# Kernel tuning notes

Measured on AMD Instinct MI355X. Metric: run time of the kernel, lower is better.

Reference implementation:

```python
import jax, jax.numpy as jnp
import numpy as np

B, T, D, H, NH = 128, 64, 64, 128, 4


def setup_inputs() -> dict:
    key = jax.random.key(0)
    ks = jax.random.split(key, 32)
    s = 0.05
    inp = {
        "x": jax.random.normal(ks[0], (B, T, D), dtype=jnp.float32),
        "mask": jnp.ones((B, T), dtype=jnp.int32),
        # per-feature GRU params (input size 1, PyTorch gate order r,z,n)
        "Wih": jax.random.normal(ks[1], (D, 3 * H), dtype=jnp.float32) * s,
        "Whh": jax.random.normal(ks[2], (D, 3 * H, H), dtype=jnp.float32) * s,
        "bih": jax.random.normal(ks[3], (D, 3 * H), dtype=jnp.float32) * s,
        "bhh": jax.random.normal(ks[4], (D, 3 * H), dtype=jnp.float32) * s,
        # MHA projections (stored [in,out]; y = x @ W + b)
        "Wq": jax.random.normal(ks[5], (H, H), dtype=jnp.float32) * s,
        "bq": jnp.zeros((H,), dtype=jnp.float32),
        "Wk": jax.random.normal(ks[6], (H, H), dtype=jnp.float32) * s,
        "bk": jnp.zeros((H,), dtype=jnp.float32),
        "Wv": jax.random.normal(ks[7], (H, H), dtype=jnp.float32) * s,
        "bv": jnp.zeros((H,), dtype=jnp.float32),
        "Wo": jax.random.normal(ks[8], (H, H), dtype=jnp.float32) * s,
        "bo": jnp.zeros((H,), dtype=jnp.float32),
        # FFN
        "W1": jax.random.normal(ks[9], (H, 2 * H), dtype=jnp.float32) * s,
        "b1": jnp.zeros((2 * H,), dtype=jnp.float32),
        "W2": jax.random.normal(ks[10], (2 * H, H), dtype=jnp.float32) * s,
        "b2": jnp.zeros((H,), dtype=jnp.float32),
        # LayerNorms
        "g1": jnp.ones((H,), dtype=jnp.float32),
        "be1": jnp.zeros((H,), dtype=jnp.float32),
        "g2": jnp.ones((H,), dtype=jnp.float32),
        "be2": jnp.zeros((H,), dtype=jnp.float32),
        # FinalAttentionQKV
        "Fq": jax.random.normal(ks[11], (H, H), dtype=jnp.float32) * s,
        "fbq": jnp.zeros((H,), dtype=jnp.float32),
        "Fk": jax.random.normal(ks[12], (H, H), dtype=jnp.float32) * s,
        "fbk": jnp.zeros((H,), dtype=jnp.float32),
        "Fv": jax.random.normal(ks[13], (H, H), dtype=jnp.float32) * s,
        "fbv": jnp.zeros((H,), dtype=jnp.float32),
        "Fout": jax.random.normal(ks[14], (H,), dtype=jnp.float32) * s,
        "fbout": jnp.zeros((), dtype=jnp.float32),
    }
    return inp


def _layernorm(x, g, b, eps=1e-5):
    m = jnp.mean(x, axis=-1, keepdims=True)
    v = jnp.mean((x - m) ** 2, axis=-1, keepdims=True)
    return (x - m) * jax.lax.rsqrt(v + eps) * g + b


def _forward(x, mask, Wih, Whh, bih, bhh, Wq, bq, Wk, bk, Wv, bv, Wo, bo,
             W1, b1, W2, b2, g1, be1, g2, be2,
             Fq, fbq, Fk, fbk, Fv, fbv, Fout, fbout):
    Bc, Tc, Dc = x.shape
    Hc = Whh.shape[-1]

    # --- D independent GRUs, fused: batch axes (B, D), scalar input per step ---
    def step(h, xt):  # h: [B,D,H], xt: [B,D]
        gx = xt[..., None] * Wih + bih                     # [B,D,3H]
        gh = jnp.einsum('bdh,dkh->bdk', h, Whh) + bhh      # [B,D,3H]
        r = jax.nn.sigmoid(gx[..., :Hc] + gh[..., :Hc])
        z = jax.nn.sigmoid(gx[..., Hc:2 * Hc] + gh[..., Hc:2 * Hc])
        n = jnp.tanh(gx[..., 2 * Hc:] + r * gh[..., 2 * Hc:])
        hn = (1.0 - z) * n + z * h
        return hn, hn

    xs = jnp.transpose(x, (1, 0, 2))                        # [T,B,D]
    h0 = jnp.zeros((Bc, Dc, Hc), dtype=x.dtype)
    _, ys = jax.lax.scan(step, h0, xs)                      # [T,B,D,H]

    # last_by_lengths: gather hidden state at index lengths-1 per batch element
    lengths = jnp.sum(mask, axis=1)                         # [B]
    idx = jnp.clip(lengths - 1, 0, Tc - 1)
    emb = ys[idx, jnp.arange(Bc)]                           # [B,D,H] (D tokens)

    # --- MHA (self-attention over D feature tokens); dropout = identity (eval) ---
    dk = Hc // NH
    def split_heads(t):
        return jnp.transpose(t.reshape(Bc, Dc, NH, dk), (0, 2, 1, 3))  # [B,NH,D,dk]
    q = split_heads(emb @ Wq + bq)
    k = split_heads(emb @ Wk + bk)
    v = split_heads(emb @ Wv + bv)
    scores = jnp.einsum('bhnd,bhmd->bhnm', q, k) / jnp.sqrt(jnp.float32(dk))
    attn = jax.nn.softmax(scores, axis=-1)
    o = jnp.einsum('bhnm,bhmd->bhnd', attn, v)
    o = jnp.transpose(o, (0, 2, 1, 3)).reshape(Bc, Dc, Hc)
    mha_out = o @ Wo + bo

    h1 = _layernorm(emb + mha_out, g1, be1)
    ffn = jax.nn.relu(h1 @ W1 + b1) @ W2 + b2
    h2 = _layernorm(h1 + ffn, g2, be2)

    # --- FinalAttentionQKV ---
    fq = (h2[:, -1, :] @ Fq + fbq)[:, None, :]              # [B,1,H]
    fk = h2 @ Fk + fbk                                      # [B,D,H]
    fv = h2 @ Fv + fbv                                      # [B,D,H]
    e = jnp.tanh(fq + fk) @ Fout + fbout                    # [B,D]
    a = jax.nn.softmax(e, axis=-1)
    return jnp.einsum('bn,bnh->bh', a, fv)                  # [B,H]


def reference(x, mask, Wih, Whh, bih, bhh, Wq, bq, Wk, bk, Wv, bv, Wo, bo,
              W1, b1, W2, b2, g1, be1, g2, be2,
              Fq, fbq, Fk, fbk, Fv, fbv, Fout, fbout):
    return _forward(x, mask, Wih, Whh, bih, bhh, Wq, bq, Wk, bk, Wv, bv, Wo, bo,
                    W1, b1, W2, b2, g1, be1, g2, be2,
                    Fq, fbq, Fk, fbk, Fv, fbv, Fout, fbout)
```

## Files before the change

kernel.cpp:

```cpp
#include <hip/hip_runtime.h>
#include <hip/hip_bf16.h>
#include <math.h>

#define BB 128
#define TT 64
#define DD 64
#define HH 128
#define NHH 4
#define K3H 384

typedef __attribute__((ext_vector_type(8))) short short8_t;
typedef __attribute__((ext_vector_type(4))) float float4_t;

#define LOG2E 1.4426950408889634f

__device__ __forceinline__ unsigned short f2bf(float f) {
    unsigned int u = __float_as_uint(f);
    u += 0x7fffu + ((u >> 16) & 1u);
    return (unsigned short)(u >> 16);
}

__device__ __forceinline__ unsigned pack_bf2(float lo, float hi) {
    return (unsigned)f2bf(lo) | ((unsigned)f2bf(hi) << 16);
}

__device__ __forceinline__ unsigned pack_bf2_hw(float lo, float hi) {
    __hip_bfloat162 p = __float22bfloat162_rn(make_float2(lo, hi));
    unsigned u;
    __builtin_memcpy(&u, &p, 4);
    return u;
}

__device__ __forceinline__ float bf2f(unsigned short s) {
    return __uint_as_float((unsigned)s << 16);
}

__device__ __forceinline__ float2 pk_fma(float2 a, float2 b, float2 c) {
    return make_float2(fmaf(a.x, b.x, c.x), fmaf(a.y, b.y, c.y));
}
__device__ __forceinline__ float2 pk_sub(float2 a, float2 b) {
    return make_float2(a.x - b.x, a.y - b.y);
}

__device__ __forceinline__ void gru_epilogue(
    const float4_t& ar, const float4_t& az, const float4_t& an, float xv,
    const float wrs[4], const float wzs[4], const float wns[4],
    const float bnis[4], float hprev[4], float hn4[4])
{
    float2 xv2 = make_float2(xv, xv);
#pragma unroll
    for (int pp = 0; pp < 2; ++pp) {
        const int r0 = 2 * pp, r1 = r0 + 1;
        float2 grs = pk_fma(xv2, make_float2(wrs[r0], wrs[r1]),
                            make_float2(ar[r0], ar[r1]));
        float2 gzs = pk_fma(xv2, make_float2(wzs[r0], wzs[r1]),
                            make_float2(az[r0], az[r1]));
        float2 rg = make_float2(
            __builtin_amdgcn_rcpf(1.f + __builtin_amdgcn_exp2f(grs.x)),
            __builtin_amdgcn_rcpf(1.f + __builtin_amdgcn_exp2f(grs.y)));
        float2 gns = pk_fma(rg, make_float2(an[r0], an[r1]),
                            pk_fma(xv2, make_float2(wns[r0], wns[r1]),
                                   make_float2(bnis[r0], bnis[r1])));
        float2 t1 = make_float2(1.f + __builtin_amdgcn_exp2f(gns.x),
                                1.f + __builtin_amdgcn_exp2f(gns.y));
        float2 t2 = make_float2(1.f + __builtin_amdgcn_exp2f(gzs.x),
                                1.f + __builtin_amdgcn_exp2f(gzs.y));
        float2 iD = make_float2(__builtin_amdgcn_rcpf(t1.x * t2.x),
                                __builtin_amdgcn_rcpf(t1.y * t2.y));
        float2 tn = make_float2(fmaf(-2.f, t2.x * iD.x, 1.f),
                                fmaf(-2.f, t2.y * iD.y, 1.f));
        float2 zg = make_float2(t1.x * iD.x, t1.y * iD.y);
        float2 hp = make_float2(hprev[r0], hprev[r1]);
        float2 hn = pk_fma(zg, pk_sub(hp, tn), tn);
        hprev[r0] = hn.x; hprev[r1] = hn.y;
        hn4[r0] = hn.x; hn4[r1] = hn.y;
    }
}

__global__ __launch_bounds__(512, 2) void gru_mfma_kernel(
    const float* __restrict__ x, const int* __restrict__ mask,
    const float* __restrict__ Wih, const float* __restrict__ Whh,
    const float* __restrict__ bih, const float* __restrict__ bhh,
    float* __restrict__ emb)
{
    const int d  = blockIdx.x;
    const int b0 = blockIdx.y * 32;
    const int tid = threadIdx.x;
    const int w = tid >> 6;
    const int l = tid & 63;
    const int m = l & 15;
    const int q = l >> 4;

    __shared__ __align__(16) unsigned short hbuf[2][2][16][144];
    __shared__ float xs_t[TT][32];
    __shared__ int tstar_s[32];
    __shared__ char lds_pad_[30 * 1024];
    if (mask[0] == 0x7abcdef) ((volatile char*)lds_pad_)[0] = 1;

    for (int idx = tid; idx < 32 * TT; idx += 512) {
        int t = idx >> 5, row = idx & 31;
        xs_t[t][row] = x[((size_t)(b0 + row) * TT + t) * DD + d];
    }
    if (tid < 32) {
        int b = b0 + tid, len = 0;
        for (int t = 0; t < TT; ++t) len += mask[b * TT + t];
        int ts = len - 1;
        if (ts < 0) ts = 0;
        if (ts > TT - 1) ts = TT - 1;
        tstar_s[tid] = ts;
    }
    for (int idx = tid; idx < 2 * 2 * 16 * 144; idx += 512)
        ((unsigned short*)hbuf)[idx] = 0;

    short8_t Wf[3][4];
#pragma unroll
    for (int g = 0; g < 3; ++g) {
        float sc = (g == 2) ? (2.f * LOG2E) : (-LOG2E);
        int kcol = g * HH + 16 * w + m;
        const float* wrow = Whh + ((size_t)d * K3H + kcol) * HH;
#pragma unroll
        for (int kc = 0; kc < 4; ++kc) {
            int j0 = kc * 32 + q * 8;
            float4 w0 = *(const float4*)(wrow + j0);
            float4 w1 = *(const float4*)(wrow + j0 + 4);
            short8_t f;
            f[0] = (short)f2bf(w0.x * sc); f[1] = (short)f2bf(w0.y * sc);
            f[2] = (short)f2bf(w0.z * sc); f[3] = (short)f2bf(w0.w * sc);
            f[4] = (short)f2bf(w1.x * sc); f[5] = (short)f2bf(w1.y * sc);
            f[6] = (short)f2bf(w1.z * sc); f[7] = (short)f2bf(w1.w * sc);
            Wf[g][kc] = f;
        }
    }

    const int hcol0 = 16 * w + q * 4;
    float4 wr4 = *(const float4*)&Wih[d * K3H + hcol0];
    float4 wz4 = *(const float4*)&Wih[d * K3H + HH + hcol0];
    float4 wn4 = *(const float4*)&Wih[d * K3H + 2 * HH + hcol0];
    float4 br4 = *(const float4*)&bih[d * K3H + hcol0];
    float4 bz4 = *(const float4*)&bih[d * K3H + HH + hcol0];
    float4 bni4 = *(const float4*)&bih[d * K3H + 2 * HH + hcol0];
    float4 bhr4 = *(const float4*)&bhh[d * K3H + hcol0];
    float4 bhz4 = *(const float4*)&bhh[d * K3H + HH + hcol0];
    float4 bnh4 = *(const float4*)&bhh[d * K3H + 2 * HH + hcol0];
    float brs[4], bzs[4], bnis[4], bnhs[4], wrs[4], wzs[4], wns[4];
#pragma unroll
    for (int r = 0; r < 4; ++r) {
        wrs[r] = -LOG2E * ((const float*)&wr4)[r];
        wzs[r] = -LOG2E * ((const float*)&wz4)[r];
        wns[r] = 2.f * LOG2E * ((const float*)&wn4)[r];
        brs[r] = -LOG2E * (((const float*)&br4)[r] + ((const float*)&bhr4)[r]);
        bzs[r] = -LOG2E * (((const float*)&bz4)[r] + ((const float*)&bhz4)[r]);
        bnis[r] = 2.f * LOG2E * ((const float*)&bni4)[r];
        bnhs[r] = 2.f * LOG2E * ((const float*)&bnh4)[r];
    }

    float hprevA[4], hprevB[4];
#pragma unroll
    for (int i = 0; i < 4; ++i) { hprevA[i] = 0.f; hprevB[i] = 0.f; }

    __syncthreads();
    const int tstarA = tstar_s[m];
    const int tstarB = tstar_s[16 + m];
    float* embpA = emb + (((size_t)(b0 + m)) * DD + d) * HH + hcol0;
    float* embpB = emb + (((size_t)(b0 + 16 + m)) * DD + d) * HH + hcol0;

    for (int t = 0; t < TT; ++t) {
        const int par = t & 1;

        short8_t hfA[4], hfB[4];
#pragma unroll
        for (int kc = 0; kc < 4; ++kc) {
            hfA[kc] = *(const short8_t*)&hbuf[0][par][m][kc * 32 + q * 8];
            hfB[kc] = *(const short8_t*)&hbuf[1][par][m][kc * 32 + q * 8];
        }
        float xvA = xs_t[t][m];
        float xvB = xs_t[t][16 + m];

        float4_t arA = {brs[0], brs[1], brs[2], brs[3]};
        float4_t azA = {bzs[0], bzs[1], bzs[2], bzs[3]};
        float4_t anA = {bnhs[0], bnhs[1], bnhs[2], bnhs[3]};
        float4_t arB = arA, azB = azA, anB = anA;
#pragma unroll
        for (int kc = 0; kc < 4; ++kc) {
            arA = __builtin_amdgcn_mfma_f32_16x16x32_bf16(Wf[0][kc], hfA[kc], arA, 0, 0, 0);
            azA = __builtin_amdgcn_mfma_f32_16x16x32_bf16(Wf[1][kc], hfA[kc], azA, 0, 0, 0);
            anA = __builtin_amdgcn_mfma_f32_16x16x32_bf16(Wf[2][kc], hfA[kc], anA, 0, 0, 0);
        }
#pragma unroll
        for (int kc = 0; kc < 4; ++kc) {
            arB = __builtin_amdgcn_mfma_f32_16x16x32_bf16(Wf[0][kc], hfB[kc], arB, 0, 0, 0);
            azB = __builtin_amdgcn_mfma_f32_16x16x32_bf16(Wf[1][kc], hfB[kc], azB, 0, 0, 0);
            anB = __builtin_amdgcn_mfma_f32_16x16x32_bf16(Wf[2][kc], hfB[kc], anB, 0, 0, 0);
        }

        float hn4[4];
        gru_epilogue(arA, azA, anA, xvA, wrs, wzs, wns, bnis, hprevA, hn4);
        {
            uint2 uu;
            uu.x = pack_bf2_hw(hn4[0], hn4[1]);
            uu.y = pack_bf2_hw(hn4[2], hn4[3]);
            *(uint2*)&hbuf[0][par ^ 1][m][hcol0] = uu;
            if (t == tstarA) {
                float4 hv; hv.x = hn4[0]; hv.y = hn4[1]; hv.z = hn4[2]; hv.w = hn4[3];
                *(float4*)embpA = hv;
            }
        }
        gru_epilogue(arB, azB, anB, xvB, wrs, wzs, wns, bnis, hprevB, hn4);
        {
            uint2 uu;
            uu.x = pack_bf2_hw(hn4[0], hn4[1]);
            uu.y = pack_bf2_hw(hn4[2], hn4[3]);
            *(uint2*)&hbuf[1][par ^ 1][m][hcol0] = uu;
            if (t == tstarB) {
                float4 hv; hv.x = hn4[0]; hv.y = hn4[1]; hv.z = hn4[2]; hv.w = hn4[3];
                *(float4*)embpB = hv;
            }
        }
        __syncthreads();
    }
}

__device__ __forceinline__ void load_wfrag(const float* __restrict__ Wp, int N,
                                           int col, float scale, int q,
                                           short8_t fr[4])
{
#pragma unroll
    for (int kc = 0; kc < 4; ++kc) {
        const float* p = Wp + (size_t)(kc * 32 + q * 8) * N + col;
        short8_t f;
#pragma unroll
        for (int j = 0; j < 8; ++j)
            f[j] = (short)f2bf(p[(size_t)j * N] * scale);
        fr[kc] = f;
    }
}

__device__ __forceinline__ void load_afrag(const unsigned short (*S)[136],
                                           short8_t Af[4][4], int m16, int q)
{
#pragma unroll
    for (int mt = 0; mt < 4; ++mt)
#pragma unroll
        for (int kc = 0; kc < 4; ++kc)
            Af[mt][kc] = *(const short8_t*)&S[mt * 16 + m16][kc * 32 + q * 8];
}

__device__ __forceinline__ void mm_regw(short8_t Af[4][4], short8_t Bf[4],
                                        float4_t acc[4])
{
#pragma unroll
    for (int mt = 0; mt < 4; ++mt) {
        float4_t a = acc[mt];
#pragma unroll
        for (int kc = 0; kc < 4; ++kc)
            a = __builtin_amdgcn_mfma_f32_16x16x32_bf16(Af[mt][kc], Bf[kc], a, 0, 0, 0);
        acc[mt] = a;
    }
}

__device__ __forceinline__ void zero4(float4_t acc[4]) {
#pragma unroll
    for (int mt = 0; mt < 4; ++mt) acc[mt] = (float4_t){0.f, 0.f, 0.f, 0.f};
}

__device__ __forceinline__ void store_rows(unsigned short (*Dst)[136], float4_t acc[4],
                                           float bv, int relu, int col, int q)
{
#pragma unroll
    for (int mt = 0; mt < 4; ++mt)
#pragma unroll
        for (int reg = 0; reg < 4; ++reg) {
            float v = acc[mt][reg] + bv;
            if (relu) v = fmaxf(v, 0.f);
            Dst[mt * 16 + q * 4 + reg][col] = f2bf(v);
        }
}

__global__ __launch_bounds__(512) void tail_kernel(
    const float* __restrict__ emb,
    const float* __restrict__ Wq, const float* __restrict__ bq,
    const float* __restrict__ Wk, const float* __restrict__ bk,
    const float* __restrict__ Wv, const float* __restrict__ bv,
    const float* __restrict__ Wo, const float* __restrict__ bo,
    const float* __restrict__ W1, const float* __restrict__ b1,
    const float* __restrict__ W2, const float* __restrict__ b2,
    const float* __restrict__ g1, const float* __restrict__ be1,
    const float* __restrict__ g2, const float* __restrict__ be2,
    const float* __restrict__ Fq, const float* __restrict__ fbq,
    const float* __restrict__ Fk, const float* __restrict__ fbk,
    const float* __restrict__ Fv, const float* __restrict__ fbv,
    const float* __restrict__ Fout, const float* __restrict__ fbout,
    float* __restrict__ out)
{
    const int b = blockIdx.x;
    const int tid = threadIdx.x;
    const int w = tid >> 6, l = tid & 63, m16 = l & 15, q = l >> 4;
    const int col = w * 16 + m16;

    __shared__ __align__(16) unsigned short E[64][136];
    __shared__ __align__(16) unsigned short Qs[64][136];
    __shared__ __align__(16) unsigned short Ks[64][136];
    __shared__ __align__(16) unsigned short Vt[128][72];
    __shared__ float sc4[4][64][66];
    __shared__ float lnp[64][8], lnp2[64][8];
    __shared__ float mean_s[64], rs_s[64];
    __shared__ float fq_s[128], fo_s[128], e_s[64], red_s[256];

    const float* embB = emb + (size_t)b * 64 * 128;
    const float SS = 0.17677669529663687f;

    short8_t WqF[4], WkF[4], WvF[4];
    load_wfrag(Wq, 128, col, SS, q, WqF);
    load_wfrag(Wk, 128, col, 1.f, q, WkF);
    load_wfrag(Wv, 128, col, 1.f, q, WvF);
    float bqv = bq[col] * SS, bkv = bk[col], bvv = bv[col];

    for (int it = tid; it < 2048; it += 512) {
        int r = it >> 5, c4 = (it & 31) << 2;
        float4 a = *(const float4*)&embB[r * 128 + c4];
        uint2 p; p.x = pack_bf2(a.x, a.y); p.y = pack_bf2(a.z, a.w);
        *(uint2*)&E[r][c4] = p;
    }
    __syncthreads();

    short8_t Af[4][4];
    float4_t acc[4];
    load_afrag(E, Af, m16, q);

    zero4(acc); mm_regw(Af, WqF, acc); store_rows(Qs, acc, bqv, 0, col, q);
    zero4(acc); mm_regw(Af, WkF, acc); store_rows(Ks, acc, bkv, 0, col, q);
    zero4(acc); mm_regw(Af, WvF, acc);
#pragma unroll
    for (int mt = 0; mt < 4; ++mt) {
        uint2 pk;
        pk.x = pack_bf2(acc[mt][0] + bvv, acc[mt][1] + bvv);
        pk.y = pack_bf2(acc[mt][2] + bvv, acc[mt][3] + bvv);
        *(uint2*)&Vt[col][mt * 16 + q * 4] = pk;
    }
    __syncthreads();

    short8_t WoF[4], W1aF[4], W1bF[4];
    load_wfrag(Wo, 128, col, 1.f, q, WoF);
    load_wfrag(W1, 256, col, 1.f, q, W1aF);
    load_wfrag(W1, 256, 128 + col, 1.f, q, W1bF);
    float bov = bo[col], b1a = b1[col], b1b = b1[128 + col];
    float g1v = g1[col], be1v = be1[col];

    {
        int hd = w >> 1, ntb = (w & 1) * 2;
#pragma unroll
        for (int mt = 0; mt < 4; ++mt) {
            short8_t Aq = *(const short8_t*)&Qs[mt * 16 + m16][hd * 32 + q * 8];
#pragma unroll
            for (int nn = 0; nn < 2; ++nn) {
                int nt = ntb + nn;
                short8_t Bk = *(const short8_t*)&Ks[nt * 16 + m16][hd * 32 + q * 8];
                float4_t a = {0.f, 0.f, 0.f, 0.f};
                a = __builtin_amdgcn_mfma_f32_16x16x32_bf16(Aq, Bk, a, 0, 0, 0);
#pragma unroll
                for (int reg = 0; reg < 4; ++reg)
                    sc4[hd][mt * 16 + q * 4 + reg][nt * 16 + m16] = a[reg];
            }
        }
    }
    __syncthreads();

    {
        int pr = tid >> 1, hd2 = pr >> 6, row = pr & 63, half = (tid & 1) * 32;
        float v[32]; float mx = -1e30f;
#pragma unroll
        for (int c = 0; c < 32; ++c) { v[c] = sc4[hd2][row][half + c]; mx = fmaxf(mx, v[c]); }
        mx = fmaxf(mx, __shfl_xor(mx, 1));
        float sum = 0.f;
#pragma unroll
        for (int c = 0; c < 32; ++c) { v[c] = __expf(v[c] - mx); sum += v[c]; }
        sum += __shfl_xor(sum, 1);
        float inv = __builtin_amdgcn_rcpf(sum);
        unsigned short (*Pd)[136] = (hd2 < 2) ? Qs : Ks;
        int cb = (hd2 & 1) * 64 + half;
#pragma unroll
        for (int c = 0; c < 16; ++c)
            *(unsigned*)&Pd[row][cb + 2 * c] = pack_bf2(v[2 * c] * inv, v[2 * c + 1] * inv);
    }
    __syncthreads();

    {
        int hd = w >> 1, nt = w & 1;
        const unsigned short (*P)[136] = (hd < 2) ? (const unsigned short (*)[136])Qs
                                                  : (const unsigned short (*)[136])Ks;
        int pb = (hd & 1) * 64;
        int vrow = hd * 32 + nt * 16 + m16;
        short8_t B0f = *(const short8_t*)&Vt[vrow][q * 8];
        short8_t B1f = *(const short8_t*)&Vt[vrow][32 + q * 8];
#pragma unroll
        for (int mt = 0; mt < 4; ++mt) {
            short8_t A0 = *(const short8_t*)&P[mt * 16 + m16][pb + q * 8];
            short8_t A1 = *(const short8_t*)&P[mt * 16 + m16][pb + 32 + q * 8];
            float4_t a = {0.f, 0.f, 0.f, 0.f};
            a = __builtin_amdgcn_mfma_f32_16x16x32_bf16(A0, B0f, a, 0, 0, 0);
            a = __builtin_amdgcn_mfma_f32_16x16x32_bf16(A1, B1f, a, 0, 0, 0);
#pragma unroll
            for (int reg = 0; reg < 4; ++reg)
                E[mt * 16 + q * 4 + reg][vrow] = f2bf(a[reg]);
        }
    }
    __syncthreads();

    short8_t W2aF[4], W2bF[4], FkF[4], FvF[4];
    load_wfrag(W2, 128, col, 1.f, q, W2aF);
    load_wfrag(W2 + (size_t)128 * 128, 128, col, 1.f, q, W2bF);
    load_wfrag(Fk, 128, col, 1.f, q, FkF);
    load_wfrag(Fv, 128, col, 1.f, q, FvF);
    float b2v = b2[col], fbkv = fbk[col], fbvv = fbv[col];
    float g2v = g2[col], be2v = be2[col];

    load_afrag(E, Af, m16, q);
    zero4(acc); mm_regw(Af, WoF, acc);
    float h1v[4][4];
#pragma unroll
    for (int mt = 0; mt < 4; ++mt)
#pragma unroll
        for (int reg = 0; reg < 4; ++reg) {
            int row = mt * 16 + q * 4 + reg;
            h1v[mt][reg] = acc[mt][reg] + bov + embB[(size_t)row * 128 + col];
        }
#pragma unroll
    for (int mt = 0; mt < 4; ++mt)
#pragma unroll
        for (int reg = 0; reg < 4; ++reg) {
            float s = h1v[mt][reg], s2 = s * s;
            s += __shfl_xor(s, 1); s += __shfl_xor(s, 2); s += __shfl_xor(s, 4); s += __shfl_xor(s, 8);
            s2 += __shfl_xor(s2, 1); s2 += __shfl_xor(s2, 2); s2 += __shfl_xor(s2, 4); s2 += __shfl_xor(s2, 8);
            if (m16 == 0) { int row = mt * 16 + q * 4 + reg; lnp[row][w] = s; lnp2[row][w] = s2; }
        }
    __syncthreads();
    if (tid < 64) {
        float s = 0.f, s2 = 0.f;
#pragma unroll
        for (int k = 0; k < 8; ++k) { s += lnp[tid][k]; s2 += lnp2[tid][k]; }
        float mn = s * (1.f / 128.f);
        mean_s[tid] = mn;
        rs_s[tid] = rsqrtf(s2 * (1.f / 128.f) - mn * mn + 1e-5f);
    }
    __syncthreads();
#pragma unroll
    for (int mt = 0; mt < 4; ++mt)
#pragma unroll
        for (int reg = 0; reg < 4; ++reg) {
            int row = mt * 16 + q * 4 + reg;
            float hv = (h1v[mt][reg] - mean_s[row]) * rs_s[row] * g1v + be1v;
            h1v[mt][reg] = hv;
            E[row][col] = f2bf(hv);
        }
    __syncthreads();

    load_afrag(E, Af, m16, q);
    zero4(acc); mm_regw(Af, W1aF, acc); store_rows(Qs, acc, b1a, 1, col, q);
    zero4(acc); mm_regw(Af, W1bF, acc); store_rows(Ks, acc, b1b, 1, col, q);
    __syncthreads();

    {
        short8_t AfQ[4][4], AfK[4][4];
        load_afrag(Qs, AfQ, m16, q);
        load_afrag(Ks, AfK, m16, q);
        zero4(acc); mm_regw(AfQ, W2aF, acc); mm_regw(AfK, W2bF, acc);
    }
#pragma unroll
    for (int mt = 0; mt < 4; ++mt)
#pragma unroll
        for (int reg = 0; reg < 4; ++reg)
            h1v[mt][reg] = acc[mt][reg] + b2v + h1v[mt][reg];
#pragma unroll
    for (int mt = 0; mt < 4; ++mt)
#pragma unroll
        for (int reg = 0; reg < 4; ++reg) {
            float s = h1v[mt][reg], s2 = s * s;
            s += __shfl_xor(s, 1); s += __shfl_xor(s, 2); s += __shfl_xor(s, 4); s += __shfl_xor(s, 8);
            s2 += __shfl_xor(s2, 1); s2 += __shfl_xor(s2, 2); s2 += __shfl_xor(s2, 4); s2 += __shfl_xor(s2, 8);
            if (m16 == 0) { int row = mt * 16 + q * 4 + reg; lnp[row][w] = s; lnp2[row][w] = s2; }
        }
    __syncthreads();
    if (tid < 64) {
        float s = 0.f, s2 = 0.f;
#pragma unroll
        for (int k = 0; k < 8; ++k) { s += lnp[tid][k]; s2 += lnp2[tid][k]; }
        float mn = s * (1.f / 128.f);
        mean_s[tid] = mn;
        rs_s[tid] = rsqrtf(s2 * (1.f / 128.f) - mn * mn + 1e-5f);
    }
    __syncthreads();
#pragma unroll
    for (int mt = 0; mt < 4; ++mt)
#pragma unroll
        for (int reg = 0; reg < 4; ++reg) {
            int row = mt * 16 + q * 4 + reg;
            float hv = (h1v[mt][reg] - mean_s[row]) * rs_s[row] * g2v + be2v;
            E[row][col] = f2bf(hv);
        }
    __syncthreads();

    load_afrag(E, Af, m16, q);
    zero4(acc); mm_regw(Af, FkF, acc); store_rows(Qs, acc, fbkv, 0, col, q);
    zero4(acc); mm_regw(Af, FvF, acc); store_rows(Ks, acc, fbvv, 0, col, q);
    {
        int co = tid >> 2, sub = tid & 3;
        float a2 = 0.f;
#pragma unroll 8
        for (int mm2 = sub * 32; mm2 < sub * 32 + 32; ++mm2)
            a2 = fmaf(bf2f(E[63][mm2]), Fq[(size_t)mm2 * 128 + co], a2);
        a2 += __shfl_xor(a2, 1);
        a2 += __shfl_xor(a2, 2);
        if (sub == 0) fq_s[co] = a2 + fbq[co];
    }
    if (tid < 128) fo_s[tid] = Fout[tid];
    __syncthreads();

    {
        int dd = tid >> 3, c8 = tid & 7;
        float p = 0.f;
#pragma unroll
        for (int c = 0; c < 16; ++c) {
            int cc = c8 * 16 + c;
            float t = fq_s[cc] + bf2f(Qs[dd][cc]);
            float tn = 1.f - 2.f * __builtin_amdgcn_rcpf(
                __builtin_amdgcn_exp2f(2.f * LOG2E * t) + 1.f);
            p = fmaf(tn, fo_s[cc], p);
        }
        p += __shfl_xor(p, 1); p += __shfl_xor(p, 2); p += __shfl_xor(p, 4);
        if (c8 == 0) e_s[dd] = p + fbout[0];
    }
    __syncthreads();
    if (tid < 64) {
        float e = e_s[tid], mx = e;
        for (int o = 32; o; o >>= 1) mx = fmaxf(mx, __shfl_xor(mx, o));
        float pe = __expf(e - mx);
        float s = pe;
        for (int o = 32; o; o >>= 1) s += __shfl_xor(s, o);
        e_s[tid] = pe / s;
    }
    __syncthreads();
    if (tid < 256) {
        int c2 = tid & 127, rg2 = tid >> 7;
        float a = 0.f;
        for (int d2 = rg2 * 32; d2 < rg2 * 32 + 32; ++d2)
            a = fmaf(e_s[d2], bf2f(Ks[d2][c2]), a);
        red_s[tid] = a;
    }
    __syncthreads();
    if (tid < 128)
        out[(size_t)b * 128 + tid] = red_s[tid] + red_s[tid + 128];
}

extern "C" void kernel_launch(void* const* d_in, const int* in_sizes, int n_in,
                              void* d_out, int out_size, void* d_ws, size_t ws_size,
                              hipStream_t stream)
{
    const float* x    = (const float*)d_in[0];
    const int*   mask = (const int*)d_in[1];
    const float* Wih  = (const float*)d_in[2];
    const float* Whh  = (const float*)d_in[3];
    const float* bih  = (const float*)d_in[4];
    const float* bhh  = (const float*)d_in[5];
    const float* Wq = (const float*)d_in[6];   const float* bq = (const float*)d_in[7];
    const float* Wk = (const float*)d_in[8];   const float* bk = (const float*)d_in[9];
    const float* Wv = (const float*)d_in[10];  const float* bv = (const float*)d_in[11];
    const float* Wo = (const float*)d_in[12];  const float* bo = (const float*)d_in[13];
    const float* W1 = (const float*)d_in[14];  const float* b1 = (const float*)d_in[15];
    const float* W2 = (const float*)d_in[16];  const float* b2 = (const float*)d_in[17];
    const float* g1 = (const float*)d_in[18];  const float* be1 = (const float*)d_in[19];
    const float* g2 = (const float*)d_in[20];  const float* be2 = (const float*)d_in[21];
    const float* Fq = (const float*)d_in[22];  const float* fbq = (const float*)d_in[23];
    const float* Fk = (const float*)d_in[24];  const float* fbk = (const float*)d_in[25];
    const float* Fv = (const float*)d_in[26];  const float* fbv = (const float*)d_in[27];
    const float* Fout = (const float*)d_in[28]; const float* fbout = (const float*)d_in[29];
    float* out = (float*)d_out;
    float* ws  = (float*)d_ws;

    float* emb = ws;

    gru_mfma_kernel<<<dim3(DD, BB / 32), 512, 0, stream>>>(x, mask, Wih, Whh, bih, bhh, emb);
    tail_kernel<<<BB, 512, 0, stream>>>(
        emb, Wq, bq, Wk, bk, Wv, bv, Wo, bo, W1, b1, W2, b2,
        g1, be1, g2, be2, Fq, fbq, Fk, fbk, Fv, fbv, Fout, fbout, out);
}
```

Before: 242.3 us.

## Software-pipeline two GRU batch halves so MFMA overlaps the other half's epilogue

Restructures the per-timestep GRU recurrence so the matrix multiply for batch half A runs while half B's gate epilogue is computed, and the reverse. Half A's MFMAs for step t+1 are issued right after A's hidden state is written, before B's epilogue. The aim is to hide MFMA latency behind the transcendental-heavy epilogue instead of running them back to back. In exchange it adds a second __syncthreads per timestep and keeps more accumulators live, which may raise register pressure.

New measurement: 244.6 us. Within noise of the previous version (+1.0%).

```diff
diff --git a/kernel.cpp b/kernel.cpp
--- a/kernel.cpp
+++ b/kernel.cpp
@@ -164,38 +164,40 @@
     float* embpA = emb + (((size_t)(b0 + m)) * DD + d) * HH + hcol0;
     float* embpB = emb + (((size_t)(b0 + 16 + m)) * DD + d) * HH + hcol0;
 
+    short8_t hfA[4];
+#pragma unroll
+    for (int kc = 0; kc < 4; ++kc)
+        hfA[kc] = *(const short8_t*)&hbuf[0][0][m][kc * 32 + q * 8];
+    float4_t arA = {brs[0], brs[1], brs[2], brs[3]};
+    float4_t azA = {bzs[0], bzs[1], bzs[2], bzs[3]};
+    float4_t anA = {bnhs[0], bnhs[1], bnhs[2], bnhs[3]};
+#pragma unroll
+    for (int kc = 0; kc < 4; ++kc) {
+        arA = __builtin_amdgcn_mfma_f32_16x16x32_bf16(Wf[0][kc], hfA[kc], arA, 0, 0, 0);
+        azA = __builtin_amdgcn_mfma_f32_16x16x32_bf16(Wf[1][kc], hfA[kc], azA, 0, 0, 0);
+        anA = __builtin_amdgcn_mfma_f32_16x16x32_bf16(Wf[2][kc], hfA[kc], anA, 0, 0, 0);
+    }
+
     for (int t = 0; t < TT; ++t) {
         const int par = t & 1;
-
-        short8_t hfA[4], hfB[4];
-#pragma unroll
-        for (int kc = 0; kc < 4; ++kc) {
-            hfA[kc] = *(const short8_t*)&hbuf[0][par][m][kc * 32 + q * 8];
-            hfB[kc] = *(const short8_t*)&hbuf[1][par][m][kc * 32 + q * 8];
-        }
-        float xvA = xs_t[t][m];
-        float xvB = xs_t[t][16 + m];
-
-        float4_t arA = {brs[0], brs[1], brs[2], brs[3]};
-        float4_t azA = {bzs[0], bzs[1], bzs[2], bzs[3]};
-        float4_t anA = {bnhs[0], bnhs[1], bnhs[2], bnhs[3]};
-        float4_t arB = arA, azB = azA, anB = anA;
-#pragma unroll
-        for (int kc = 0; kc < 4; ++kc) {
-            arA = __builtin_amdgcn_mfma_f32_16x16x32_bf16(Wf[0][kc], hfA[kc], arA, 0, 0, 0);
-            azA = __builtin_amdgcn_mfma_f32_16x16x32_bf16(Wf[1][kc], hfA[kc], azA, 0, 0, 0);
-            anA = __builtin_amdgcn_mfma_f32_16x16x32_bf16(Wf[2][kc], hfA[kc], anA, 0, 0, 0);
-        }
-#pragma unroll
-        for (int kc = 0; kc < 4; ++kc) {
-            arB = __builtin_amdgcn_mfma_f32_16x16x32_bf16(Wf[0][kc], hfB[kc], arB, 0, 0, 0);
-            azB = __builtin_amdgcn_mfma_f32_16x16x32_bf16(Wf[1][kc], hfB[kc], azB, 0, 0, 0);
-            anB = __builtin_amdgcn_mfma_f32_16x16x32_bf16(Wf[2][kc], hfB[kc], anB, 0, 0, 0);
-        }
-
         float hn4[4];
-        gru_epilogue(arA, azA, anA, xvA, wrs, wzs, wns, bnis, hprevA, hn4);
+
         {
+            short8_t hfB[4];
+#pragma unroll
+            for (int kc = 0; kc < 4; ++kc)
+                hfB[kc] = *(const short8_t*)&hbuf[1][par][m][kc * 32 + q * 8];
+            float4_t arB = {brs[0], brs[1], brs[2], brs[3]};
+            float4_t azB = {bzs[0], bzs[1], bzs[2], bzs[3]};
+            float4_t anB = {bnhs[0], bnhs[1], bnhs[2], bnhs[3]};
+#pragma unroll
+            for (int kc = 0; kc < 4; ++kc) {
+                arB = __builtin_amdgcn_mfma_f32_16x16x32_bf16(Wf[0][kc], hfB[kc], arB, 0, 0, 0);
+                azB = __builtin_amdgcn_mfma_f32_16x16x32_bf16(Wf[1][kc], hfB[kc], azB, 0, 0, 0);
+                anB = __builtin_amdgcn_mfma_f32_16x16x32_bf16(Wf[2][kc], hfB[kc], anB, 0, 0, 0);
+            }
+
+            gru_epilogue(arA, azA, anA, xs_t[t][m], wrs, wzs, wns, bnis, hprevA, hn4);
             uint2 uu;
             uu.x = pack_bf2_hw(hn4[0], hn4[1]);
             uu.y = pack_bf2_hw(hn4[2], hn4[3]);
@@ -204,10 +206,24 @@
                 float4 hv; hv.x = hn4[0]; hv.y = hn4[1]; hv.z = hn4[2]; hv.w = hn4[3];
                 *(float4*)embpA = hv;
             }
-        }
-        gru_epilogue(arB, azB, anB, xvB, wrs, wzs, wns, bnis, hprevB, hn4);
-        {
-            uint2 uu;
+            __syncthreads();
+
+            if (t < TT - 1) {
+#pragma unroll
+                for (int kc = 0; kc < 4; ++kc)
+                    hfA[kc] = *(const short8_t*)&hbuf[0][par ^ 1][m][kc * 32 + q * 8];
+                arA = (float4_t){brs[0], brs[1], brs[2], brs[3]};
+                azA = (float4_t){bzs[0], bzs[1], bzs[2], bzs[3]};
+                anA = (float4_t){bnhs[0], bnhs[1], bnhs[2], bnhs[3]};
+#pragma unroll
+                for (int kc = 0; kc < 4; ++kc) {
+                    arA = __builtin_amdgcn_mfma_f32_16x16x32_bf16(Wf[0][kc], hfA[kc], arA, 0, 0, 0);
+                    azA = __builtin_amdgcn_mfma_f32_16x16x32_bf16(Wf[1][kc], hfA[kc], azA, 0, 0, 0);
+                    anA = __builtin_amdgcn_mfma_f32_16x16x32_bf16(Wf[2][kc], hfA[kc], anA, 0, 0, 0);
+                }
+            }
+
+            gru_epilogue(arB, azB, anB, xs_t[t][16 + m], wrs, wzs, wns, bnis, hprevB, hn4);
             uu.x = pack_bf2_hw(hn4[0], hn4[1]);
             uu.y = pack_bf2_hw(hn4[2], hn4[3]);
             *(uint2*)&hbuf[1][par ^ 1][m][hcol0] = uu;
@@ -215,8 +231,8 @@
                 float4 hv; hv.x = hn4[0]; hv.y = hn4[1]; hv.z = hn4[2]; hv.w = hn4[3];
                 *(float4*)embpB = hv;
             }
-        }
-        __syncthreads();
+            __syncthreads();
+        }
     }
 }
 
```
